# Kernel tuning notes

Hardware: AMD Instinct MI355X
Metric: run time of the kernel (lower is better)

The kernel has to match this reference:

```python
import jax, jax.numpy as jnp
import numpy as np

DIM = 3
N_GRID = 128
DX = 1.0 / N_GRID
INV_DX = float(N_GRID)
DT = 1e-4
P_VOL = (DX * 0.5) ** 2
P_RHO = 1.0
P_MASS = P_VOL * P_RHO
E_MOD = 5000.0
NU = 0.2
MU0 = E_MOD / (2.0 * (1.0 + NU))
LAM0 = E_MOD * NU / ((1.0 + NU) * (1.0 - 2.0 * NU))
N_PARTICLES = 400_000

# 27 stencil offsets of the quadratic B-spline kernel
_OFF = jnp.array([[i, j, k] for i in range(3) for j in range(3) for k in range(3)],
                 dtype=jnp.int32)  # [27,3]


def _substep(x, v, C, F, Jp, gravity, attractor_strength, attractor_pos, material):
    N = x.shape[0]
    dtype = x.dtype
    I3 = jnp.eye(3, dtype=dtype)

    # ---- particle -> grid (P2G) ----
    base = jnp.floor(x * INV_DX - 0.5).astype(jnp.int32)          # [N,3]
    fx = x * INV_DX - base.astype(dtype)                          # [N,3]
    # quadratic kernel weights, w[a, n, d], a in {0,1,2}
    w = jnp.stack([0.5 * (1.5 - fx) ** 2,
                   0.75 - (fx - 1.0) ** 2,
                   0.5 * (fx - 0.5) ** 2], axis=0)                # [3,N,3]

    Fn = jnp.einsum('nij,njk->nik', I3 + DT * C, F)               # deformation update

    h = jnp.clip(jnp.exp(10.0 * (1.0 - Jp)), 0.1, 5.0)
    h = jnp.where(material == 1, 0.3, h)
    mu = jnp.where(material == 0, 0.0, MU0 * h)                   # [N]
    la = LAM0 * h                                                 # [N]

    U, s, Vh = jnp.linalg.svd(Fn, full_matrices=False)            # [N,3,3],[N,3],[N,3,3]

    # faithful to source: plasticity loop only touches first TWO singular values
    J = jnp.ones_like(Jp)
    sig = s
    for d in range(2):
        new_sig = jnp.where(material == 2,
                            jnp.clip(s[:, d], 1.0 - 0.025, 1.0 + 0.0045),
                            s[:, d])
        Jp = Jp * s[:, d] / new_sig
        sig = sig.at[:, d].set(new_sig)
        J = J * new_sig

    F_fluid = jnp.sqrt(J)[:, None, None] * I3                     # material 0
    F_snow = jnpum = None
    F_snow = jnp.einsum('nij,nj,njk->nik', U, sig, Vh)            # material 2: U diag(sig) V^T
    m3 = material[:, None, None]
    Fn = jnp.where(m3 == 0, F_fluid, jnp.where(m3 == 2, F_snow, Fn))

    R = jnp.einsum('nij,njk->nik', U, Vh)                         # U V^T (rotation)
    stress = (2.0 * mu[:, None, None] * jnp.einsum('nij,nkj->nik', Fn - R, Fn)
              + I3 * (la * J * (J - 1.0))[:, None, None])
    stress = (-DT * P_VOL * 4.0 * INV_DX * INV_DX) * stress
    affine = stress + P_MASS * C                                  # [N,3,3]

    # NOTE faithful quirk of the source: weight = w[i][0] * w[j][1] (k-component unused)
    weight = w[_OFF[:, 0], :, 0] * w[_OFF[:, 1], :, 1]            # [27,N]
    dpos = (_OFF[:, None, :].astype(dtype) - fx[None]) * DX       # [27,N,3]
    mom = weight[..., None] * (P_MASS * v[None]
                               + jnp.einsum('nij,onj->oni', affine, dpos))  # [27,N,3]

    idx = base[None] + _OFF[:, None, :]                           # [27,N,3]
    flat = (idx[..., 0] * N_GRID + idx[..., 1]) * N_GRID + idx[..., 2]      # [27,N]
    G3 = N_GRID ** 3
    grid_mom = jnp.zeros((G3, 3), dtype).at[flat.reshape(-1)].add(mom.reshape(-1, 3))
    grid_m = jnp.zeros((G3,), dtype).at[flat.reshape(-1)].add((weight * P_MASS).reshape(-1))

    # ---- grid update ----
    a = jnp.arange(N_GRID, dtype=jnp.int32)
    coords = jnp.stack(jnp.meshgrid(a, a, a, indexing='ij'), axis=-1).reshape(G3, 3)
    mask = grid_m > 0
    m_safe = jnp.where(mask, grid_m, 1.0)
    gv = grid_mom / m_safe[:, None]
    gv = gv + DT * gravity * 30.0
    dist = attractor_pos[None, :] - DX * coords.astype(dtype)
    gv = gv + dist / (0.01 + jnp.linalg.norm(dist, axis=-1, keepdims=True)) \
              * attractor_strength * DT * 100.0
    ic, jc = coords[:, 0], coords[:, 1]
    vx, vy, vz = gv[:, 0], gv[:, 1], gv[:, 2]
    vx = jnp.where((ic < 3) & (vx < 0), 0.0, vx)
    vx = jnp.where((ic > N_GRID - 3) & (vx > 0), 0.0, vx)
    vy = jnp.where((jc < 3) & (vy < 0), 0.0, vy)
    vy = jnp.where((jc > N_GRID - 3) & (vy > 0), 0.0, vy)
    gv = jnp.stack([vx, vy, vz], axis=-1)
    gv = jnp.where(mask[:, None], gv, 0.0)                        # untouched cells stay zero

    # ---- grid -> particle (G2P) ----
    g_v = gv[flat]                                                # [27,N,3]
    dpos2 = _OFF[:, None, :].astype(dtype) - fx[None]             # [27,N,3] (no dx scale)
    new_v = jnp.einsum('on,onc->nc', weight, g_v)                 # [N,3]
    new_C = 4.0 * INV_DX * jnp.einsum('on,onc,ond->ncd', weight, g_v, dpos2)  # [N,3,3]
    x_new = x + DT * new_v

    # pack state: [x(3) | v(3) | Jp(1) | F(9) | C(9)] -> [N,25]
    return jnp.concatenate([x_new, new_v, Jp[:, None],
                            Fn.reshape(N, 9), new_C.reshape(N, 9)], axis=1)


def setup_inputs() -> dict:
    key = jax.random.key(0)
    ks = jax.random.split(key, 9)
    N = N_PARTICLES
    x = 0.1 + 0.8 * jax.random.uniform(ks[0], (N, 3), dtype=jnp.float32)
    v = 0.1 * jax.random.normal(ks[1], (N, 3), dtype=jnp.float32)
    C = 0.01 * jax.random.normal(ks[2], (N, 3, 3), dtype=jnp.float32)
    F = jnp.eye(3, dtype=jnp.float32) + 0.01 * jax.random.normal(ks[3], (N, 3, 3), dtype=jnp.float32)
    Jp = 1.0 + 0.1 * jax.random.uniform(ks[4], (N,), dtype=jnp.float32)
    material = jax.random.randint(ks[5], (N,), 0, 3, dtype=jnp.int32)
    gravity = jnp.array([0.0, -1.0, 0.0], dtype=jnp.float32)
    attractor_strength = jax.random.uniform(ks[6], (), dtype=jnp.float32)
    attractor_pos = jax.random.uniform(ks[7], (3,), dtype=jnp.float32)
    return {"x": x, "v": v, "C": C, "F": F, "Jp": Jp,
            "gravity": gravity, "attractor_strength": attractor_strength,
            "attractor_pos": attractor_pos, "material": material}


def reference(x, v, C, F, Jp, gravity, attractor_strength, attractor_pos, material):
    return _substep(x, v, C, F, Jp, gravity, attractor_strength, attractor_pos, material)
```

## Files before the change

kernel.cpp:

```cpp
#include <hip/hip_runtime.h>

#define NG 128
#define G3 (NG*NG*NG)
#define NSCAN_BLOCKS (G3/256)

__device__ __constant__ const float c_DX      = 1.0f/128.0f;
__device__ __constant__ const float c_INV_DX  = 128.0f;

#define DT      1e-4f
#define P_VOL   ((1.0f/256.0f)*(1.0f/256.0f))
#define P_MASS  P_VOL
#define MU0     (5000.0f/(2.0f*1.2f))
#define LAM0    (5000.0f*0.2f/(1.2f*0.6f))

struct __align__(16) PRec {
    float4 r0, r1, r2, r3;
};

__device__ inline void jacobi_rot(float S[3][3], float V[3][3], int p, int q) {
    float apq = S[p][q];
    if (fabsf(apq) < 1e-24f) return;
    float tau = (S[q][q] - S[p][p]) / (2.0f * apq);
    float t = copysignf(1.0f, tau) / (fabsf(tau) + sqrtf(1.0f + tau*tau));
    float c = rsqrtf(1.0f + t*t);
    float sn = t * c;
    #pragma unroll
    for (int k = 0; k < 3; ++k) {
        float Spk = S[p][k], Sqk = S[q][k];
        S[p][k] = c*Spk - sn*Sqk;
        S[q][k] = sn*Spk + c*Sqk;
    }
    #pragma unroll
    for (int k = 0; k < 3; ++k) {
        float Skp = S[k][p], Skq = S[k][q];
        S[k][p] = c*Skp - sn*Skq;
        S[k][q] = sn*Skp + c*Skq;
    }
    #pragma unroll
    for (int k = 0; k < 3; ++k) {
        float Vkp = V[k][p], Vkq = V[k][q];
        V[k][p] = c*Vkp - sn*Vkq;
        V[k][q] = sn*Vkp + c*Vkq;
    }
}

__device__ inline void svd3(const float A[9], float U[9], float sv[3], float V[9]) {
    float S[3][3];
    #pragma unroll
    for (int i = 0; i < 3; ++i)
        #pragma unroll
        for (int j = 0; j < 3; ++j) {
            float acc = 0.f;
            #pragma unroll
            for (int k = 0; k < 3; ++k) acc += A[k*3+i]*A[k*3+j];
            S[i][j] = acc;
        }
    float Vm[3][3] = {{1.f,0.f,0.f},{0.f,1.f,0.f},{0.f,0.f,1.f}};
    #pragma unroll
    for (int sweep = 0; sweep < 4; ++sweep) {
        jacobi_rot(S, Vm, 0, 1);
        jacobi_rot(S, Vm, 0, 2);
        jacobi_rot(S, Vm, 1, 2);
    }
    float lam[3] = {S[0][0], S[1][1], S[2][2]};
    int i0 = 0, i1 = 1, i2 = 2, t;
    if (lam[i0] < lam[i1]) { t = i0; i0 = i1; i1 = t; }
    if (lam[i0] < lam[i2]) { t = i0; i0 = i2; i2 = t; }
    if (lam[i1] < lam[i2]) { t = i1; i1 = i2; i2 = t; }
    int ord[3] = {i0, i1, i2};
    #pragma unroll
    for (int c = 0; c < 3; ++c) {
        int s_ = ord[c];
        float l = fmaxf(lam[s_], 0.f);
        float sval = sqrtf(l);
        sv[c] = sval;
        float v0 = Vm[0][s_], v1 = Vm[1][s_], v2 = Vm[2][s_];
        V[0*3+c] = v0; V[1*3+c] = v1; V[2*3+c] = v2;
        float inv = (sval > 1e-12f) ? 1.0f/sval : 0.f;
        U[0*3+c] = (A[0]*v0 + A[1]*v1 + A[2]*v2)*inv;
        U[1*3+c] = (A[3]*v0 + A[4]*v1 + A[5]*v2)*inv;
        U[2*3+c] = (A[6]*v0 + A[7]*v1 + A[8]*v2)*inv;
    }
}

__device__ inline void base_from_A(float A0, float A1, float A2,
                                   int& bi, int& bj, int& bk,
                                   float& fx0, float& fx1, float& fx2) {
    float bxf = floorf(A0 - 0.5f);
    float byf = floorf(A1 - 0.5f);
    float bzf = floorf(A2 - 0.5f);
    bi = (int)bxf; bj = (int)byf; bk = (int)bzf;
    bi = min(max(bi, 0), NG-3); bj = min(max(bj, 0), NG-3); bk = min(max(bk, 0), NG-3);
    fx0 = A0 - bxf;
    fx1 = A1 - byf;
    fx2 = A2 - bzf;
}

__global__ void __launch_bounds__(256)
count_kernel(const float* __restrict__ x, int* __restrict__ cell_count,
             int* __restrict__ rank, int N) {
    int n = blockIdx.x*256 + threadIdx.x;
    if (n >= N) return;
    int bi, bj, bk; float f0, f1, f2;
    base_from_A(x[3*n+0]*c_INV_DX, x[3*n+1]*c_INV_DX, x[3*n+2]*c_INV_DX,
                bi, bj, bk, f0, f1, f2);
    rank[n] = atomicAdd(&cell_count[(bi*NG + bj)*NG + bk], 1);
}

__global__ void __launch_bounds__(256)
scan_partial_kernel(const int* __restrict__ count, int* __restrict__ partial) {
    __shared__ int red[256];
    int t = threadIdx.x;
    red[t] = count[blockIdx.x*256 + t];
    __syncthreads();
    for (int off = 128; off > 0; off >>= 1) {
        if (t < off) red[t] += red[t+off];
        __syncthreads();
    }
    if (t == 0) partial[blockIdx.x] = red[0];
}

__global__ void __launch_bounds__(256)
scan_partials_kernel(int* __restrict__ partial) {
    __shared__ int part[256];
    int t = threadIdx.x;
    int base = t*32;
    int local[32];
    int s = 0;
    #pragma unroll
    for (int i = 0; i < 32; ++i) { local[i] = s; s += partial[base+i]; }
    part[t] = s;
    __syncthreads();
    for (int off = 1; off < 256; off <<= 1) {
        int v = (t >= off) ? part[t-off] : 0;
        __syncthreads();
        part[t] += v;
        __syncthreads();
    }
    int prev = (t == 0) ? 0 : part[t-1];
    #pragma unroll
    for (int i = 0; i < 32; ++i) partial[base+i] = prev + local[i];
}

__global__ void __launch_bounds__(256)
scan_final_kernel(const int* __restrict__ count, const int* __restrict__ partial,
                  int* __restrict__ offset) {
    __shared__ int part[256];
    int t = threadIdx.x;
    int i = blockIdx.x*256 + t;
    int c = count[i];
    part[t] = c;
    __syncthreads();
    for (int off = 1; off < 256; off <<= 1) {
        int v = (t >= off) ? part[t-off] : 0;
        __syncthreads();
        part[t] += v;
        __syncthreads();
    }
    int base = partial[blockIdx.x];
    offset[i] = base + part[t] - c;
    if (i == G3-1) offset[G3] = base + part[t];
}

__global__ void __launch_bounds__(256)
pre_kernel(const float* __restrict__ x, const float* __restrict__ v,
           const float* __restrict__ Cin, const float* __restrict__ Fin,
           const float* __restrict__ Jp_in, const int* __restrict__ material,
           const int* __restrict__ offset, const int* __restrict__ rank,
           PRec* __restrict__ rec, float* __restrict__ out, int N) {
    int n = blockIdx.x*256 + threadIdx.x;
    if (n >= N) return;

    float A0 = x[3*n+0]*c_INV_DX, A1 = x[3*n+1]*c_INV_DX, A2 = x[3*n+2]*c_INV_DX;
    int bi, bj, bk; float f0, f1, f2;
    base_from_A(A0, A1, A2, bi, bj, bk, f0, f1, f2);

    float Cm[9], Fm[9];
    #pragma unroll
    for (int i = 0; i < 9; ++i) { Cm[i] = Cin[9*n+i]; Fm[i] = Fin[9*n+i]; }

    float Fn[9];
    #pragma unroll
    for (int i = 0; i < 3; ++i)
        #pragma unroll
        for (int k = 0; k < 3; ++k) {
            float acc = Fm[i*3+k];
            #pragma unroll
            for (int j = 0; j < 3; ++j) acc += DT * Cm[i*3+j] * Fm[j*3+k];
            Fn[i*3+k] = acc;
        }

    float Jp = Jp_in[n];
    int mat = material[n];
    float h = expf(10.0f*(1.0f - Jp));
    h = fminf(fmaxf(h, 0.1f), 5.0f);
    if (mat == 1) h = 0.3f;
    float mu = (mat == 0) ? 0.0f : MU0*h;
    float la = LAM0*h;

    float U[9], V[9], sv[3];
    svd3(Fn, U, sv, V);

    float J = 1.0f;
    float sig[3];
    #pragma unroll
    for (int d = 0; d < 2; ++d) {
        float s = sv[d];
        float ns = (mat == 2) ? fminf(fmaxf(s, 1.0f-0.025f), 1.0f+0.0045f) : s;
        Jp = Jp * s / ns;
        sig[d] = ns;
        J *= ns;
    }
    sig[2] = sv[2];

    if (mat == 0) {
        float sj = sqrtf(J);
        Fn[0]=sj; Fn[1]=0; Fn[2]=0; Fn[3]=0; Fn[4]=sj; Fn[5]=0; Fn[6]=0; Fn[7]=0; Fn[8]=sj;
    } else if (mat == 2) {
        #pragma unroll
        for (int i = 0; i < 3; ++i)
            #pragma unroll
            for (int k = 0; k < 3; ++k) {
                float acc = 0.f;
                #pragma unroll
                for (int j = 0; j < 3; ++j) acc += U[i*3+j]*sig[j]*V[k*3+j];
                Fn[i*3+k] = acc;
            }
    }

    float R[9];
    #pragma unroll
    for (int i = 0; i < 3; ++i)
        #pragma unroll
        for (int k = 0; k < 3; ++k) {
            float acc = 0.f;
            #pragma unroll
            for (int j = 0; j < 3; ++j) acc += U[i*3+j]*V[k*3+j];
            R[i*3+k] = acc;
        }

    float press = la * J * (J - 1.0f);
    float scale = -DT * P_VOL * 4.0f * c_INV_DX * c_INV_DX;
    float aff[9];
    #pragma unroll
    for (int i = 0; i < 3; ++i)
        #pragma unroll
        for (int k = 0; k < 3; ++k) {
            float acc = 0.f;
            #pragma unroll
            for (int j = 0; j < 3; ++j) acc += (Fn[i*3+j]-R[i*3+j])*Fn[k*3+j];
            acc = 2.0f*mu*acc;
            if (i == k) acc += press;
            aff[i*3+k] = scale*acc + P_MASS*Cm[i*3+k];
        }

    float* po = out + (size_t)n*25;
    po[6] = Jp;
    #pragma unroll
    for (int i = 0; i < 9; ++i) po[7+i] = Fn[i];

    int cell = (bi*NG + bj)*NG + bk;
    int pos = offset[cell] + rank[n];

    float4* rp = (float4*)&rec[pos];
    rp[0] = make_float4(A0, A1, A2, __int_as_float(n));
    rp[1] = make_float4(aff[0], aff[1], aff[2], aff[3]);
    rp[2] = make_float4(aff[4], aff[5], aff[6], aff[7]);
    rp[3] = make_float4(aff[8], P_MASS*v[3*n+0], P_MASS*v[3*n+1], P_MASS*v[3*n+2]);
}

__global__ void __launch_bounds__(256)
grid_gather_kernel(const PRec* __restrict__ rec, const int* __restrict__ offset,
                   float4* __restrict__ grid, const float* __restrict__ gravity,
                   const float* __restrict__ attr_s, const float* __restrict__ attr_p) {
    int g4 = blockIdx.x*256 + threadIdx.x;
    int zq = g4 & 31;
    int gj = (g4 >> 5) & (NG-1);
    int gi = g4 >> 12;
    int zlo = zq*4;

    float ax[4], ay[4], az[4], mm[4];
    #pragma unroll
    for (int h = 0; h < 4; ++h) { ax[h]=0.f; ay[h]=0.f; az[h]=0.f; mm[h]=0.f; }

    int bi0 = max(gi-2, 0), bi1 = min(gi, NG-3);
    int bj0 = max(gj-2, 0), bj1 = min(gj, NG-3);
    int bk0 = max(zlo-2, 0), bk1 = min(zlo+3, NG-3);

    float gif = (float)gi, gjf = (float)gj, z0f = (float)zlo;
    bool any = false;

    for (int bi = bi0; bi <= bi1; ++bi) {
        for (int bj = bj0; bj <= bj1; ++bj) {
            int col = (bi*NG + bj)*NG;
            int s = offset[col + bk0];
            int e = offset[col + bk1 + 1];
            if (s < e) any = true;
            for (int p = s; p < e; ++p) {
                const float4* rp = (const float4*)&rec[p];
                float4 r0 = rp[0];
                float4 r1 = rp[1];
                float4 r2 = rp[2];
                float4 r3 = rp[3];

                float ux = gif - r0.x;
                float aux = fabsf(ux);
                float tx = 1.5f - aux;
                float nx = (aux < 0.5f) ? (0.75f - ux*ux) : (0.5f*tx*tx);
                float uy = gjf - r0.y;
                float auy = fabsf(uy);
                float ty = 1.5f - auy;
                float ny = (auy < 0.5f) ? (0.75f - uy*uy) : (0.5f*ty*ty);
                float wgt = nx*ny;

                float uz0 = z0f - r0.z;
                float dpx = ux*c_DX, dpy = uy*c_DX, dpz0 = uz0*c_DX;
                float cx = r3.y + r1.x*dpx + r1.y*dpy + r1.z*dpz0;
                float cy = r3.z + r1.w*dpx + r2.x*dpy + r2.y*dpz0;
                float cz = r3.w + r2.z*dpx + r2.w*dpy + r3.x*dpz0;
                float ix = r1.z*c_DX, iy = r2.y*c_DX, iz = r3.x*c_DX;

                #pragma unroll
                for (int h = 0; h < 4; ++h) {
                    float uz = uz0 + (float)h;
                    float w = (uz > -1.5f && uz <= 1.5f) ? wgt : 0.f;
                    ax[h] += w*cx; ay[h] += w*cy; az[h] += w*cz; mm[h] += w*P_MASS;
                    cx += ix; cy += iy; cz += iz;
                }
            }
        }
    }

    if (!any) return;

    float gx = DT*gravity[0]*30.0f, gy = DT*gravity[1]*30.0f, gz = DT*gravity[2]*30.0f;
    float apx = attr_p[0], apy = attr_p[1], apz = attr_p[2];
    float as  = attr_s[0] * DT * 100.0f;

    int gidx = (gi*NG + gj)*NG + zlo;
    #pragma unroll
    for (int h = 0; h < 4; ++h) {
        float m = mm[h];
        int gk = zlo + h;
        float gvx = 0.f, gvy = 0.f, gvz = 0.f;
        if (m > 0.f) {
            float inv = 1.0f/m;
            gvx = ax[h]*inv + gx; gvy = ay[h]*inv + gy; gvz = az[h]*inv + gz;
            float dx_ = apx - c_DX*(float)gi;
            float dy_ = apy - c_DX*(float)gj;
            float dz_ = apz - c_DX*(float)gk;
            float nrm = sqrtf(dx_*dx_ + dy_*dy_ + dz_*dz_);
            float sc = as / (0.01f + nrm);
            gvx += dx_*sc; gvy += dy_*sc; gvz += dz_*sc;
            if (gi < 3      && gvx < 0.f) gvx = 0.f;
            if (gi > NG-3   && gvx > 0.f) gvx = 0.f;
            if (gj < 3      && gvy < 0.f) gvy = 0.f;
            if (gj > NG-3   && gvy > 0.f) gvy = 0.f;
        }
        grid[gidx + h] = make_float4(gvx, gvy, gvz, m);
    }
}

__global__ void __launch_bounds__(256)
g2p_kernel(const PRec* __restrict__ rec, const float4* __restrict__ grid,
           float* __restrict__ out, int N) {
    int gid = blockIdx.x * 256 + threadIdx.x;
    if (gid >= N) return;

    float4 r0 = rec[gid].r0;
    float A0 = r0.x, A1 = r0.y, A2 = r0.z;
    int n = __float_as_int(r0.w);

    int bi, bj, bk; float fx0, fx1, fx2;
    base_from_A(A0, A1, A2, bi, bj, bk, fx0, fx1, fx2);

    float wx[3], wy[3];
    wx[0] = 0.5f*(1.5f-fx0)*(1.5f-fx0); wx[1] = 0.75f-(fx0-1.f)*(fx0-1.f); wx[2] = 0.5f*(fx0-0.5f)*(fx0-0.5f);
    wy[0] = 0.5f*(1.5f-fx1)*(1.5f-fx1); wy[1] = 0.75f-(fx1-1.f)*(fx1-1.f); wy[2] = 0.5f*(fx1-0.5f)*(fx1-0.5f);

    float nvx = 0.f, nvy = 0.f, nvz = 0.f;
    float nC[9];
    #pragma unroll
    for (int i = 0; i < 9; ++i) nC[i] = 0.f;

    #pragma unroll
    for (int i = 0; i < 3; ++i) {
        float dpx = (float)i - fx0;
        #pragma unroll
        for (int j = 0; j < 3; ++j) {
            float wgt = wx[i]*wy[j];
            float dpy = (float)j - fx1;
            int cell0 = ((bi+i)*NG + (bj+j))*NG + bk;
            #pragma unroll
            for (int k = 0; k < 3; ++k) {
                float dpz = (float)k - fx2;
                float4 gv = grid[cell0 + k];
                float wgx = wgt*gv.x, wgy = wgt*gv.y, wgz = wgt*gv.z;
                nvx += wgx; nvy += wgy; nvz += wgz;
                nC[0] += wgx*dpx; nC[1] += wgx*dpy; nC[2] += wgx*dpz;
                nC[3] += wgy*dpx; nC[4] += wgy*dpy; nC[5] += wgy*dpz;
                nC[6] += wgz*dpx; nC[7] += wgz*dpy; nC[8] += wgz*dpz;
            }
        }
    }

    float* po = out + (size_t)n*25;
    float px = A0*c_DX, py = A1*c_DX, pz = A2*c_DX;
    po[0] = px + DT*nvx;
    po[1] = py + DT*nvy;
    po[2] = pz + DT*nvz;
    po[3] = nvx; po[4] = nvy; po[5] = nvz;
    float s4 = 4.0f*c_INV_DX;
    #pragma unroll
    for (int i = 0; i < 9; ++i) po[16+i] = s4*nC[i];
}

extern "C" void kernel_launch(void* const* d_in, const int* in_sizes, int n_in,
                              void* d_out, int out_size, void* d_ws, size_t ws_size,
                              hipStream_t stream) {
    const float* x        = (const float*)d_in[0];
    const float* v        = (const float*)d_in[1];
    const float* C        = (const float*)d_in[2];
    const float* F        = (const float*)d_in[3];
    const float* Jp       = (const float*)d_in[4];
    const float* gravity  = (const float*)d_in[5];
    const float* attr_s   = (const float*)d_in[6];
    const float* attr_p   = (const float*)d_in[7];
    const int*   material = (const int*)d_in[8];
    float* out = (float*)d_out;
    int N = in_sizes[0] / 3;

    char* ws = (char*)d_ws;
    size_t o = 0;
    int* cell_count = (int*)(ws + o);      o += (size_t)G3*sizeof(int);
    size_t zero_bytes = o;
    int* offset     = (int*)(ws + o);      o += ((size_t)G3+1)*sizeof(int);
    int* partial    = (int*)(ws + o);      o += (size_t)NSCAN_BLOCKS*sizeof(int);
    int* rank       = (int*)(ws + o);      o += (size_t)N*sizeof(int);
    o = (o + 127) & ~(size_t)127;
    float4* grid    = (float4*)(ws + o);   o += (size_t)G3*sizeof(float4);
    PRec* rec       = (PRec*)(ws + o);     o += (size_t)N*sizeof(PRec);

    hipMemsetAsync(d_ws, 0, zero_bytes, stream);

    int pblocks = (N + 255) / 256;
    count_kernel<<<pblocks, 256, 0, stream>>>(x, cell_count, rank, N);
    scan_partial_kernel<<<NSCAN_BLOCKS, 256, 0, stream>>>(cell_count, partial);
    scan_partials_kernel<<<1, 256, 0, stream>>>(partial);
    scan_final_kernel<<<NSCAN_BLOCKS, 256, 0, stream>>>(cell_count, partial, offset);
    pre_kernel<<<pblocks, 256, 0, stream>>>(x, v, C, F, Jp, material,
                                            offset, rank, rec, out, N);
    grid_gather_kernel<<<G3/1024, 256, 0, stream>>>(rec, offset, grid,
                                                    gravity, attr_s, attr_p);
    g2p_kernel<<<pblocks, 256, 0, stream>>>(rec, grid, out, N);
}
```

Measured before the change: 280.8 us.

## Replace per-cell gather P2G with tiled LDS-atomic scatter per 4x4 column block

The grid-centric gather, where each thread scans every neighbouring particle column, is replaced by a block-per-4x4-(i,j)-tile kernel. Each block streams the particles in the overlapping columns and scatters their 27-point stencil contributions into a shared-memory accumulator of full z columns using LDS atomics, then normalises and writes the grid. This cuts the redundant particle reads and weight evaluations repeated across neighbouring gather threads. The cost is heavy shared-memory atomic contention, 32 KB of LDS per block, and halo particles being processed by up to four blocks.

```diff
diff --git a/kernel.cpp b/kernel.cpp
--- a/kernel.cpp
+++ b/kernel.cpp
@@ -12,6 +12,9 @@
 #define P_MASS  P_VOL
 #define MU0     (5000.0f/(2.0f*1.2f))
 #define LAM0    (5000.0f*0.2f/(1.2f*0.6f))
+
+#define TI 4
+#define TJ 4
 
 struct __align__(16) PRec {
     float4 r0, r1, r2, r3;
@@ -270,82 +273,104 @@
 }
 
 __global__ void __launch_bounds__(256)
-grid_gather_kernel(const PRec* __restrict__ rec, const int* __restrict__ offset,
+p2g_scatter_kernel(const PRec* __restrict__ rec, const int* __restrict__ offset,
                    float4* __restrict__ grid, const float* __restrict__ gravity,
                    const float* __restrict__ attr_s, const float* __restrict__ attr_p) {
-    int g4 = blockIdx.x*256 + threadIdx.x;
-    int zq = g4 & 31;
-    int gj = (g4 >> 5) & (NG-1);
-    int gi = g4 >> 12;
-    int zlo = zq*4;
-
-    float ax[4], ay[4], az[4], mm[4];
-    #pragma unroll
-    for (int h = 0; h < 4; ++h) { ax[h]=0.f; ay[h]=0.f; az[h]=0.f; mm[h]=0.f; }
-
-    int bi0 = max(gi-2, 0), bi1 = min(gi, NG-3);
-    int bj0 = max(gj-2, 0), bj1 = min(gj, NG-3);
-    int bk0 = max(zlo-2, 0), bk1 = min(zlo+3, NG-3);
-
-    float gif = (float)gi, gjf = (float)gj, z0f = (float)zlo;
-    bool any = false;
-
-    for (int bi = bi0; bi <= bi1; ++bi) {
-        for (int bj = bj0; bj <= bj1; ++bj) {
-            int col = (bi*NG + bj)*NG;
-            int s = offset[col + bk0];
-            int e = offset[col + bk1 + 1];
-            if (s < e) any = true;
-            for (int p = s; p < e; ++p) {
-                const float4* rp = (const float4*)&rec[p];
-                float4 r0 = rp[0];
-                float4 r1 = rp[1];
-                float4 r2 = rp[2];
-                float4 r3 = rp[3];
-
-                float ux = gif - r0.x;
-                float aux = fabsf(ux);
-                float tx = 1.5f - aux;
-                float nx = (aux < 0.5f) ? (0.75f - ux*ux) : (0.5f*tx*tx);
-                float uy = gjf - r0.y;
-                float auy = fabsf(uy);
-                float ty = 1.5f - auy;
-                float ny = (auy < 0.5f) ? (0.75f - uy*uy) : (0.5f*ty*ty);
-                float wgt = nx*ny;
-
-                float uz0 = z0f - r0.z;
-                float dpx = ux*c_DX, dpy = uy*c_DX, dpz0 = uz0*c_DX;
-                float cx = r3.y + r1.x*dpx + r1.y*dpy + r1.z*dpz0;
-                float cy = r3.z + r1.w*dpx + r2.x*dpy + r2.y*dpz0;
-                float cz = r3.w + r2.z*dpx + r2.w*dpy + r3.x*dpz0;
-                float ix = r1.z*c_DX, iy = r2.y*c_DX, iz = r3.x*c_DX;
-
+    __shared__ float4 acc4[TI*TJ*NG];
+    float* acc = (float*)acc4;
+
+    int t = threadIdx.x;
+    int gi0 = (int)(blockIdx.x >> 5) * TI;
+    int gj0 = (int)(blockIdx.x & 31) * TJ;
+
+    int bi_lo = max(gi0-2, 0), bi_hi = min(gi0+TI-1, NG-3);
+    int bj_lo = max(gj0-2, 0), bj_hi = min(gj0+TJ-1, NG-3);
+
+    int total = 0;
+    for (int bi = bi_lo; bi <= bi_hi; ++bi)
+        total += offset[(bi*NG + bj_hi)*NG + NG] - offset[(bi*NG + bj_lo)*NG];
+    if (total == 0) return;
+
+    #pragma unroll
+    for (int i = 0; i < (TI*TJ*NG)/256; ++i)
+        acc4[t + i*256] = make_float4(0.f, 0.f, 0.f, 0.f);
+    __syncthreads();
+
+    for (int bi = bi_lo; bi <= bi_hi; ++bi) {
+        int s = offset[(bi*NG + bj_lo)*NG];
+        int e = offset[(bi*NG + bj_hi)*NG + NG];
+        for (int p = s + t; p < e; p += 256) {
+            const float4* rp = (const float4*)&rec[p];
+            float4 r0 = rp[0];
+            float4 r1 = rp[1];
+            float4 r2 = rp[2];
+            float4 r3 = rp[3];
+
+            int pbi, pbj, pbk; float f0, f1, f2;
+            base_from_A(r0.x, r0.y, r0.z, pbi, pbj, pbk, f0, f1, f2);
+
+            float wx[3], wy[3];
+            wx[0] = 0.5f*(1.5f-f0)*(1.5f-f0);
+            wx[1] = 0.75f-(f0-1.f)*(f0-1.f);
+            wx[2] = 0.5f*(f0-0.5f)*(f0-0.5f);
+            wy[0] = 0.5f*(1.5f-f1)*(1.5f-f1);
+            wy[1] = 0.75f-(f1-1.f)*(f1-1.f);
+            wy[2] = 0.5f*(f1-0.5f)*(f1-0.5f);
+
+            float dpx[3] = {(0.f-f0)*c_DX, (1.f-f0)*c_DX, (2.f-f0)*c_DX};
+            float dpy[3] = {(0.f-f1)*c_DX, (1.f-f1)*c_DX, (2.f-f1)*c_DX};
+            float dpz[3] = {(0.f-f2)*c_DX, (1.f-f2)*c_DX, (2.f-f2)*c_DX};
+
+            int li = pbi - gi0;
+            int lj = pbj - gj0;
+
+            #pragma unroll
+            for (int di = 0; di < 3; ++di) {
+                int ci = li + di;
+                if ((unsigned)ci >= TI) continue;
                 #pragma unroll
-                for (int h = 0; h < 4; ++h) {
-                    float uz = uz0 + (float)h;
-                    float w = (uz > -1.5f && uz <= 1.5f) ? wgt : 0.f;
-                    ax[h] += w*cx; ay[h] += w*cy; az[h] += w*cz; mm[h] += w*P_MASS;
-                    cx += ix; cy += iy; cz += iz;
+                for (int dj = 0; dj < 3; ++dj) {
+                    int cj = lj + dj;
+                    if ((unsigned)cj >= TJ) continue;
+                    float w2 = wx[di]*wy[dj];
+                    float wm = w2 * P_MASS;
+                    float bx = r3.y + r1.x*dpx[di] + r1.y*dpy[dj];
+                    float by = r3.z + r1.w*dpx[di] + r2.x*dpy[dj];
+                    float bz = r3.w + r2.z*dpx[di] + r2.w*dpy[dj];
+                    int bidx = ((ci*TJ + cj)*NG + pbk)*4;
+                    #pragma unroll
+                    for (int dk = 0; dk < 3; ++dk) {
+                        float dz = dpz[dk];
+                        atomicAdd(&acc[bidx + 4*dk + 0], w2*(bx + r1.z*dz));
+                        atomicAdd(&acc[bidx + 4*dk + 1], w2*(by + r2.y*dz));
+                        atomicAdd(&acc[bidx + 4*dk + 2], w2*(bz + r3.x*dz));
+                        atomicAdd(&acc[bidx + 4*dk + 3], wm);
+                    }
                 }
             }
         }
     }
-
-    if (!any) return;
+    __syncthreads();
 
     float gx = DT*gravity[0]*30.0f, gy = DT*gravity[1]*30.0f, gz = DT*gravity[2]*30.0f;
     float apx = attr_p[0], apy = attr_p[1], apz = attr_p[2];
     float as  = attr_s[0] * DT * 100.0f;
 
-    int gidx = (gi*NG + gj)*NG + zlo;
-    #pragma unroll
-    for (int h = 0; h < 4; ++h) {
-        float m = mm[h];
-        int gk = zlo + h;
+    #pragma unroll
+    for (int it = 0; it < (TI*TJ*NG)/256; ++it) {
+        int cidx = t + it*256;
+        int lz   = cidx & (NG-1);
+        int pair = cidx >> 7;
+        int lj   = pair & (TJ-1);
+        int li   = pair >> 2;
+        int gi = gi0 + li, gj = gj0 + lj, gk = lz;
+
+        float4 a4 = acc4[cidx];
+        float m = a4.w;
         float gvx = 0.f, gvy = 0.f, gvz = 0.f;
         if (m > 0.f) {
             float inv = 1.0f/m;
-            gvx = ax[h]*inv + gx; gvy = ay[h]*inv + gy; gvz = az[h]*inv + gz;
+            gvx = a4.x*inv + gx; gvy = a4.y*inv + gy; gvz = a4.z*inv + gz;
             float dx_ = apx - c_DX*(float)gi;
             float dy_ = apy - c_DX*(float)gj;
             float dz_ = apz - c_DX*(float)gk;
@@ -357,7 +382,7 @@
             if (gj < 3      && gvy < 0.f) gvy = 0.f;
             if (gj > NG-3   && gvy > 0.f) gvy = 0.f;
         }
-        grid[gidx + h] = make_float4(gvx, gvy, gvz, m);
+        grid[(gi*NG + gj)*NG + gk] = make_float4(gvx, gvy, gvz, m);
     }
 }
 
@@ -450,7 +475,7 @@
     scan_final_kernel<<<NSCAN_BLOCKS, 256, 0, stream>>>(cell_count, partial, offset);
     pre_kernel<<<pblocks, 256, 0, stream>>>(x, v, C, F, Jp, material,
                                             offset, rank, rec, out, N);
-    grid_gather_kernel<<<G3/1024, 256, 0, stream>>>(rec, offset, grid,
-                                                    gravity, attr_s, attr_p);
+    p2g_scatter_kernel<<<(NG/TI)*(NG/TJ), 256, 0, stream>>>(rec, offset, grid,
+                                                            gravity, attr_s, attr_p);
     g2p_kernel<<<pblocks, 256, 0, stream>>>(rec, grid, out, N);
 }
```

Result: slower. 553.0 us (+96.9%).
